# Optimization experiments

Measured on AMD Instinct MI355X. Metric: run time of the kernel, lower is better.

## Reference

```python
import jax, jax.numpy as jnp
import numpy as np

B, N, D = 4, 4096, 128
H = 128  # hidden_size == input_size (required by residual add)

def setup_inputs() -> dict:
    key = jax.random.key(0)
    kx, kw, kb = jax.random.split(key, 3)
    x = jax.random.normal(kx, (B, N, D), dtype=jnp.float32)
    # nn.Linear(input_size, hidden_size): weight [H, D], bias [H]
    lim = 1.0 / np.sqrt(D)
    W = jax.random.uniform(kw, (H, D), dtype=jnp.float32, minval=-lim, maxval=lim)
    b = jax.random.uniform(kb, (H,), dtype=jnp.float32, minval=-lim, maxval=lim)
    return {"x": x, "W": W, "b": b}

def reference(x, W, b):
    # adj[b,i,j] = <x[b,i], x[b,j]>, relu
    adj = jax.nn.relu(jnp.einsum('bid,bjd->bij', x, x))  # [B,N,N]
    # torch sums over dim=1 (rows) -> per-column sums, then divides columns
    col_sum = adj.sum(axis=1)                 # [B,N]
    adj = adj / col_sum[:, None, :]           # broadcast over dim 1
    out = jnp.einsum('bij,bjd->bid', adj, x)  # aggregate
    out = jnp.tanh(jnp.einsum('bnd,hd->bnh', out, W) + b)
    # Dropout(0.5) treated as eval-mode identity
    return out + x  # residual=True
```

## Files before the change

kernel.cpp:

```cpp
#include <hip/hip_runtime.h>
#include <hip/hip_bf16.h>

#define BN 4
#define NN 4096
#define DD 128

typedef __attribute__((ext_vector_type(8))) __bf16 bf16x8;
typedef __attribute__((ext_vector_type(4))) float f32x4;

typedef union {
  bf16x8 v;
  unsigned int u[4];
  uint2 u2[2];
} pk8;

typedef __attribute__((address_space(1))) const unsigned int* gas_p;
typedef __attribute__((address_space(3))) unsigned int* las_p;

__device__ __forceinline__ void gload16(const void* g, void* l) {
  __builtin_amdgcn_global_load_lds((gas_p)g, (las_p)l, 16, 0, 0);
}
__device__ __forceinline__ void wait_vm0() {
  asm volatile("s_waitcnt vmcnt(0)" ::: "memory");
}
__device__ __forceinline__ void wait_vm4() {
  asm volatile("s_waitcnt vmcnt(4)" ::: "memory");
}
__device__ __forceinline__ unsigned int cvtpk(float lo, float hi) {
  unsigned int r;
  asm("v_cvt_pk_bf16_f32 %0, %1, %2" : "=v"(r) : "v"(lo), "v"(hi));
  return r;
}
__device__ __forceinline__ unsigned int pkrelu(float lo, float hi) {
  return cvtpk(fmaxf(lo, 0.f), fmaxf(hi, 0.f));
}

__device__ inline unsigned short f2bf(float f) {
  unsigned int u = __float_as_uint(f);
  unsigned int r = (u + 0x7FFFu + ((u >> 16) & 1u)) >> 16;
  return (unsigned short)r;
}
__device__ inline float bf2f(unsigned short s) {
  return __uint_as_float(((unsigned int)s) << 16);
}

__global__ __launch_bounds__(256) void k_cvt(const float* __restrict__ x,
                                             unsigned short* __restrict__ xb) {
  int i = (blockIdx.x * 256 + threadIdx.x) * 8;
  float4 a = *(const float4*)(x + i);
  float4 c = *(const float4*)(x + i + 4);
  uint4 o;
  o.x = cvtpk(a.x, a.y);
  o.y = cvtpk(a.z, a.w);
  o.z = cvtpk(c.x, c.y);
  o.w = cvtpk(c.z, c.w);
  *(uint4*)(xb + i) = o;
}

__global__ __launch_bounds__(256, 4) void k_colsum(const unsigned short* __restrict__ xb,
                                                   float* __restrict__ colpart) {
  __shared__ unsigned short XiB[2][64 * 128];
  const int b = blockIdx.y, j0 = blockIdx.x * 128, ic = blockIdx.z;
  const int tid = threadIdx.x, lane = tid & 63, wv = tid >> 6;
  const unsigned short* xbb = xb + b * NN * DD;
  const int g = lane >> 4;
  const int ibeg = ic * (NN / 8);
  const int nt = (NN / 8) / 64;

#pragma unroll
  for (int hb = 0; hb < 2; ++hb)
#pragma unroll
    for (int q = 0; q < 4; ++q) {
      int c = wv * 4 + q;
      int lr = c * 4 + g;
      int gsrc = (lane & 15) ^ (lr & 7);
      gload16(&xbb[(j0 + hb * 64 + lr) * 128 + gsrc * 8], &XiB[hb][c * 512]);
    }
  wait_vm0();
  __syncthreads();

  bf16x8 bfr[2][4];
#pragma unroll
  for (int ni = 0; ni < 2; ++ni)
#pragma unroll
    for (int kk = 0; kk < 4; ++kk) {
      int lr = (wv & 1) * 32 + ni * 16 + (lane & 15);
      bfr[ni][kk] = *(const bf16x8*)&XiB[wv >> 1][lr * 128 + (((kk * 4 + g) ^ (lr & 7)) << 3)];
    }
  __syncthreads();

#pragma unroll
  for (int q = 0; q < 4; ++q) {
    int c = wv * 4 + q;
    int lr = c * 4 + g;
    int gsrc = (lane & 15) ^ (lr & 7);
    gload16(&xbb[(ibeg + lr) * 128 + gsrc * 8], &XiB[1][c * 512]);
  }

  int basek[4];
#pragma unroll
  for (int kk = 0; kk < 4; ++kk)
    basek[kk] = (lane & 15) * 128 + (((kk * 4 + g) ^ (lane & 7)) << 3);

  float colacc0 = 0.f, colacc1 = 0.f;
  for (int t = 0; t < nt; ++t) {
    wait_vm0();
    __syncthreads();
    const int cur = (t + 1) & 1, nxt = t & 1;
    if (t + 1 < nt) {
      const int i1 = ibeg + (t + 1) * 64;
#pragma unroll
      for (int q = 0; q < 4; ++q) {
        int c = wv * 4 + q;
        int lr = c * 4 + g;
        int gsrc = (lane & 15) ^ (lr & 7);
        gload16(&xbb[(i1 + lr) * 128 + gsrc * 8], &XiB[nxt][c * 512]);
      }
    }
    f32x4 a0[4], a1[4];
#pragma unroll
    for (int mj = 0; mj < 4; ++mj) { a0[mj] = (f32x4){}; a1[mj] = (f32x4){}; }
    __builtin_amdgcn_s_setprio(1);
#pragma unroll
    for (int kk = 0; kk < 4; ++kk) {
      bf16x8 ar0 = *(const bf16x8*)&XiB[cur][basek[kk]];
      bf16x8 ar1 = *(const bf16x8*)&XiB[cur][basek[kk] + 1 * 2048];
      bf16x8 ar2 = *(const bf16x8*)&XiB[cur][basek[kk] + 2 * 2048];
      bf16x8 ar3 = *(const bf16x8*)&XiB[cur][basek[kk] + 3 * 2048];
      a0[0] = __builtin_amdgcn_mfma_f32_16x16x32_bf16(ar0, bfr[0][kk], a0[0], 0, 0, 0);
      a1[0] = __builtin_amdgcn_mfma_f32_16x16x32_bf16(ar0, bfr[1][kk], a1[0], 0, 0, 0);
      a0[1] = __builtin_amdgcn_mfma_f32_16x16x32_bf16(ar1, bfr[0][kk], a0[1], 0, 0, 0);
      a1[1] = __builtin_amdgcn_mfma_f32_16x16x32_bf16(ar1, bfr[1][kk], a1[1], 0, 0, 0);
      a0[2] = __builtin_amdgcn_mfma_f32_16x16x32_bf16(ar2, bfr[0][kk], a0[2], 0, 0, 0);
      a1[2] = __builtin_amdgcn_mfma_f32_16x16x32_bf16(ar2, bfr[1][kk], a1[2], 0, 0, 0);
      a0[3] = __builtin_amdgcn_mfma_f32_16x16x32_bf16(ar3, bfr[0][kk], a0[3], 0, 0, 0);
      a1[3] = __builtin_amdgcn_mfma_f32_16x16x32_bf16(ar3, bfr[1][kk], a1[3], 0, 0, 0);
    }
    __builtin_amdgcn_s_setprio(0);
    {
      float s0 = 0.f, s1 = 0.f;
#pragma unroll
      for (int mj = 0; mj < 4; ++mj)
#pragma unroll
        for (int r = 0; r < 4; ++r) {
          s0 += fmaxf(a0[mj][r], 0.f);
          s1 += fmaxf(a1[mj][r], 0.f);
        }
      s0 += __shfl_xor(s0, 16); s0 += __shfl_xor(s0, 32);
      s1 += __shfl_xor(s1, 16); s1 += __shfl_xor(s1, 32);
      colacc0 += s0; colacc1 += s1;
    }
  }
  if (lane < 16) {
    colpart[(ic * BN + b) * NN + j0 + wv * 32 + lane] = colacc0;
    colpart[(ic * BN + b) * NN + j0 + wv * 32 + 16 + lane] = colacc1;
  }
}

__global__ __launch_bounds__(256) void k_ytrans(const float* __restrict__ x,
                                                const float* __restrict__ colpart,
                                                unsigned short* __restrict__ yt) {
  __shared__ unsigned short T[64 * 72];
  const int b = blockIdx.z, j0 = blockIdx.y * 64, d0 = blockIdx.x * 64;
  const int tid = threadIdx.x;
  int jr = tid >> 2, q0 = (tid & 3) * 16;
  float cs = 0.f;
#pragma unroll
  for (int ic = 0; ic < 8; ++ic) cs += colpart[(ic * BN + b) * NN + j0 + jr];
  float inv = 1.0f / cs;
  const float* xr = x + (size_t)(b * NN + j0 + jr) * DD + d0 + q0;
#pragma unroll
  for (int q = 0; q < 4; ++q) {
    float4 v = *(const float4*)(xr + q * 4);
    int dc = q0 + q * 4;
    T[jr * 72 + dc + 0] = f2bf(v.x * inv);
    T[jr * 72 + dc + 1] = f2bf(v.y * inv);
    T[jr * 72 + dc + 2] = f2bf(v.z * inv);
    T[jr * 72 + dc + 3] = f2bf(v.w * inv);
  }
  __syncthreads();
  for (int c = tid; c < 512; c += 256) {
    int dr = c >> 3, jg = c & 7;
    alignas(16) unsigned short tmp[8];
#pragma unroll
    for (int u = 0; u < 8; ++u) tmp[u] = T[(jg * 8 + u) * 72 + dr];
    *(uint4*)&yt[(size_t)(b * DD + d0 + dr) * NN + j0 + jg * 8] = *(const uint4*)tmp;
  }
}

__global__ __launch_bounds__(256, 2) void k_pass2(const unsigned short* __restrict__ xb,
                                                  const unsigned short* __restrict__ yt,
                                                  unsigned short* __restrict__ opart,
                                                  int jc) {
  __shared__ unsigned short XjB[2][64 * 128];
  __shared__ unsigned short YsB[3][128 * 64];
  const int b = blockIdx.y, i0 = blockIdx.x * 128, zc = blockIdx.z;
  const int tid = threadIdx.x, lane = tid & 63, wv = tid >> 6;
  const unsigned short* xbb = xb + b * NN * DD;
  const unsigned short* ytb = yt + (size_t)b * DD * NN;
  const int g = lane >> 4, l15 = lane & 15;

  const int jspan = NN / jc;
  const int jbeg = zc * jspan;
  const int nt = jspan / 64;

#pragma unroll
  for (int hb = 0; hb < 2; ++hb)
#pragma unroll
    for (int q = 0; q < 4; ++q) {
      int c = wv * 4 + q;
      int lr = c * 4 + g;
      int gsrc = l15 ^ (lr & 7);
      gload16(&xbb[(i0 + hb * 64 + lr) * 128 + gsrc * 8], &XjB[hb][c * 512]);
    }
  wait_vm0();
  __syncthreads();

  bf16x8 bfr[2][4];
#pragma unroll
  for (int ni = 0; ni < 2; ++ni)
#pragma unroll
    for (int kk = 0; kk < 4; ++kk) {
      int lr = (wv & 1) * 32 + ni * 16 + l15;
      bfr[ni][kk] = *(const bf16x8*)&XjB[wv >> 1][lr * 128 + (((kk * 4 + g) ^ (lr & 7)) << 3)];
    }
  __syncthreads();

#pragma unroll
  for (int q = 0; q < 4; ++q) {
    int c = wv * 4 + q;
    int lr = c * 4 + g;
    int gsrc = l15 ^ (lr & 7);
    gload16(&xbb[(jbeg + lr) * 128 + gsrc * 8], &XjB[0][c * 512]);
  }
#pragma unroll
  for (int q = 0; q < 4; ++q) {
    int c = wv * 4 + q;
    int dr = c * 8 + (lane >> 3);
    int gsrc = (lane & 7) ^ (dr & 7);
    gload16(&ytb[(size_t)dr * NN + jbeg + gsrc * 8], &YsB[0][c * 512]);
  }
  if (1 < nt) {
#pragma unroll
    for (int q = 0; q < 4; ++q) {
      int c = wv * 4 + q;
      int dr = c * 8 + (lane >> 3);
      int gsrc = (lane & 7) ^ (dr & 7);
      gload16(&ytb[(size_t)dr * NN + jbeg + 64 + gsrc * 8], &YsB[1][c * 512]);
    }
  }

  int xjb[4];
#pragma unroll
  for (int kk = 0; kk < 4; ++kk)
    xjb[kk] = l15 * 128 + (((kk * 4 + g) ^ (lane & 7)) << 3);
  int ysb[2][2];
#pragma unroll
  for (int c = 0; c < 2; ++c)
#pragma unroll
    for (int h = 0; h < 2; ++h) {
      int jq = c * 4 + 2 * h + (g >> 1);
      ysb[c][h] = l15 * 64 + ((jq ^ (l15 & 7)) << 3) + (g & 1) * 4;
    }

  f32x4 oacc0[8], oacc1[8];
#pragma unroll
  for (int n = 0; n < 8; ++n) { oacc0[n] = (f32x4){}; oacc1[n] = (f32x4){}; }

  int ybuf = 0;
  for (int t = 0; t < nt; ++t) {
    if (t + 1 < nt) wait_vm4(); else wait_vm0();
    __syncthreads();
    if (t + 1 < nt) {
      const int j1 = jbeg + (t + 1) * 64;
#pragma unroll
      for (int q = 0; q < 4; ++q) {
        int c = wv * 4 + q;
        int lr = c * 4 + g;
        int gsrc = l15 ^ (lr & 7);
        gload16(&xbb[(j1 + lr) * 128 + gsrc * 8], &XjB[(t + 1) & 1][c * 512]);
      }
      if (t + 2 < nt) {
        const int j2 = jbeg + (t + 2) * 64;
        int nb = ybuf + 2; if (nb >= 3) nb -= 3;
#pragma unroll
        for (int q = 0; q < 4; ++q) {
          int c = wv * 4 + q;
          int dr = c * 8 + (lane >> 3);
          int gsrc = (lane & 7) ^ (dr & 7);
          gload16(&ytb[(size_t)dr * NN + j2 + gsrc * 8], &YsB[nb][c * 512]);
        }
      }
    }
    const unsigned short* Xj = XjB[t & 1];
    const unsigned short* Ys = YsB[ybuf];

    f32x4 s0[4], s1[4];
#pragma unroll
    for (int mj = 0; mj < 4; ++mj) { s0[mj] = (f32x4){}; s1[mj] = (f32x4){}; }
    __builtin_amdgcn_s_setprio(1);
#pragma unroll
    for (int kk = 0; kk < 4; ++kk) {
      bf16x8 ar0 = *(const bf16x8*)&Xj[xjb[kk]];
      bf16x8 ar1 = *(const bf16x8*)&Xj[xjb[kk] + 1 * 2048];
      bf16x8 ar2 = *(const bf16x8*)&Xj[xjb[kk] + 2 * 2048];
      bf16x8 ar3 = *(const bf16x8*)&Xj[xjb[kk] + 3 * 2048];
      s0[0] = __builtin_amdgcn_mfma_f32_16x16x32_bf16(ar0, bfr[0][kk], s0[0], 0, 0, 0);
      s1[0] = __builtin_amdgcn_mfma_f32_16x16x32_bf16(ar0, bfr[1][kk], s1[0], 0, 0, 0);
      s0[1] = __builtin_amdgcn_mfma_f32_16x16x32_bf16(ar1, bfr[0][kk], s0[1], 0, 0, 0);
      s1[1] = __builtin_amdgcn_mfma_f32_16x16x32_bf16(ar1, bfr[1][kk], s1[1], 0, 0, 0);
      s0[2] = __builtin_amdgcn_mfma_f32_16x16x32_bf16(ar2, bfr[0][kk], s0[2], 0, 0, 0);
      s1[2] = __builtin_amdgcn_mfma_f32_16x16x32_bf16(ar2, bfr[1][kk], s1[2], 0, 0, 0);
      s0[3] = __builtin_amdgcn_mfma_f32_16x16x32_bf16(ar3, bfr[0][kk], s0[3], 0, 0, 0);
      s1[3] = __builtin_amdgcn_mfma_f32_16x16x32_bf16(ar3, bfr[1][kk], s1[3], 0, 0, 0);
    }
    __builtin_amdgcn_s_setprio(0);
    pk8 p00, p01, p10, p11;
    p00.u[0] = pkrelu(s0[0][0], s0[0][1]); p00.u[1] = pkrelu(s0[0][2], s0[0][3]);
    p00.u[2] = pkrelu(s0[1][0], s0[1][1]); p00.u[3] = pkrelu(s0[1][2], s0[1][3]);
    p01.u[0] = pkrelu(s1[0][0], s1[0][1]); p01.u[1] = pkrelu(s1[0][2], s1[0][3]);
    p01.u[2] = pkrelu(s1[1][0], s1[1][1]); p01.u[3] = pkrelu(s1[1][2], s1[1][3]);
    p10.u[0] = pkrelu(s0[2][0], s0[2][1]); p10.u[1] = pkrelu(s0[2][2], s0[2][3]);
    p10.u[2] = pkrelu(s0[3][0], s0[3][1]); p10.u[3] = pkrelu(s0[3][2], s0[3][3]);
    p11.u[0] = pkrelu(s1[2][0], s1[2][1]); p11.u[1] = pkrelu(s1[2][2], s1[2][3]);
    p11.u[2] = pkrelu(s1[3][0], s1[3][1]); p11.u[3] = pkrelu(s1[3][2], s1[3][3]);
    __builtin_amdgcn_s_setprio(1);
#pragma unroll
    for (int n = 0; n < 8; ++n) {
      pk8 bb0, bb1;
      bb0.u2[0] = *(const uint2*)&Ys[ysb[0][0] + n * 1024];
      bb0.u2[1] = *(const uint2*)&Ys[ysb[0][1] + n * 1024];
      bb1.u2[0] = *(const uint2*)&Ys[ysb[1][0] + n * 1024];
      bb1.u2[1] = *(const uint2*)&Ys[ysb[1][1] + n * 1024];
      oacc0[n] = __builtin_amdgcn_mfma_f32_16x16x32_bf16(p00.v, bb0.v, oacc0[n], 0, 0, 0);
      oacc1[n] = __builtin_amdgcn_mfma_f32_16x16x32_bf16(p01.v, bb0.v, oacc1[n], 0, 0, 0);
      oacc0[n] = __builtin_amdgcn_mfma_f32_16x16x32_bf16(p10.v, bb1.v, oacc0[n], 0, 0, 0);
      oacc1[n] = __builtin_amdgcn_mfma_f32_16x16x32_bf16(p11.v, bb1.v, oacc1[n], 0, 0, 0);
    }
    __builtin_amdgcn_s_setprio(0);
    ++ybuf; if (ybuf == 3) ybuf = 0;
  }

  __syncthreads();
  unsigned short* sb = &XjB[0][0];
#pragma unroll
  for (int m = 0; m < 2; ++m)
#pragma unroll
    for (int n = 0; n < 8; ++n)
#pragma unroll
      for (int r = 0; r < 4; ++r) {
        int row = wv * 32 + m * 16 + g * 4 + r;
        int col = n * 16 + l15;
        sb[row * 128 + col] = f2bf(m == 0 ? oacc0[n][r] : oacc1[n][r]);
      }
  __syncthreads();
  for (int c = tid; c < 2048; c += 256) {
    int row = c >> 4, gq = c & 15;
    *(uint4*)&opart[((size_t)zc * (BN * NN) + b * NN + i0 + row) * DD + gq * 8] =
        *(const uint4*)&sb[row * 128 + gq * 8];
  }
}

__global__ __launch_bounds__(256) void k_final(const unsigned short* __restrict__ opart,
                                               int jc,
                                               const float* __restrict__ W,
                                               const float* __restrict__ bias,
                                               const float* __restrict__ x,
                                               float* __restrict__ out) {
  __shared__ unsigned short Wb[128 * 128];
  __shared__ unsigned short PreS[32 * 128];
  const int tid = threadIdx.x, lane = tid & 63, wv = tid >> 6;
  const int g = lane >> 4;
  const int r0 = blockIdx.x * 32;

  {
    int h = tid >> 1, k0h = (tid & 1) * 8;
    const float* wr = W + h * 128 + k0h * 8;
#pragma unroll
    for (int q = 0; q < 8; ++q) {
      float4 v0 = *(const float4*)(wr + q * 8);
      float4 v1 = *(const float4*)(wr + q * 8 + 4);
      uint4 o;
      o.x = cvtpk(v0.x, v0.y); o.y = cvtpk(v0.z, v0.w);
      o.z = cvtpk(v1.x, v1.y); o.w = cvtpk(v1.z, v1.w);
      int gq = k0h + q;
      *(uint4*)&Wb[h * 128 + ((gq ^ (h & 7)) << 3)] = o;
    }
  }
  for (int c = tid; c < 512; c += 256) {
    int row = c >> 4, gq = c & 15;
    float s[8] = {0.f, 0.f, 0.f, 0.f, 0.f, 0.f, 0.f, 0.f};
    for (int ch = 0; ch < jc; ++ch) {
      uint4 pk = *(const uint4*)&opart[((size_t)ch * (BN * NN) + r0 + row) * DD + gq * 8];
      alignas(16) unsigned short us[8];
      *(uint4*)us = pk;
#pragma unroll
      for (int u = 0; u < 8; ++u) s[u] += bf2f(us[u]);
    }
    uint4 o;
    o.x = cvtpk(s[0], s[1]); o.y = cvtpk(s[2], s[3]);
    o.z = cvtpk(s[4], s[5]); o.w = cvtpk(s[6], s[7]);
    *(uint4*)&PreS[row * 128 + ((gq ^ (row & 7)) << 3)] = o;
  }
  __syncthreads();

  bf16x8 af[2][4], bf[2][4];
#pragma unroll
  for (int m = 0; m < 2; ++m)
#pragma unroll
    for (int kk = 0; kk < 4; ++kk) {
      int row = m * 16 + (lane & 15);
      af[m][kk] = *(const bf16x8*)&PreS[row * 128 + (((kk * 4 + g) ^ (row & 7)) << 3)];
    }
#pragma unroll
  for (int n = 0; n < 2; ++n)
#pragma unroll
    for (int kk = 0; kk < 4; ++kk) {
      int h = wv * 32 + n * 16 + (lane & 15);
      bf[n][kk] = *(const bf16x8*)&Wb[h * 128 + (((kk * 4 + g) ^ (h & 7)) << 3)];
    }

  f32x4 acc[2][2] = {};
#pragma unroll
  for (int kk = 0; kk < 4; ++kk) {
    acc[0][0] = __builtin_amdgcn_mfma_f32_16x16x32_bf16(af[0][kk], bf[0][kk], acc[0][0], 0, 0, 0);
    acc[0][1] = __builtin_amdgcn_mfma_f32_16x16x32_bf16(af[0][kk], bf[1][kk], acc[0][1], 0, 0, 0);
    acc[1][0] = __builtin_amdgcn_mfma_f32_16x16x32_bf16(af[1][kk], bf[0][kk], acc[1][0], 0, 0, 0);
    acc[1][1] = __builtin_amdgcn_mfma_f32_16x16x32_bf16(af[1][kk], bf[1][kk], acc[1][1], 0, 0, 0);
  }

  float bh0 = bias[wv * 32 + (lane & 15)];
  float bh1 = bias[wv * 32 + 16 + (lane & 15)];
#pragma unroll
  for (int m = 0; m < 2; ++m)
#pragma unroll
    for (int n = 0; n < 2; ++n)
#pragma unroll
      for (int r = 0; r < 4; ++r) {
        int row = r0 + m * 16 + g * 4 + r;
        int h = wv * 32 + n * 16 + (lane & 15);
        size_t idx = (size_t)row * 128 + h;
        out[idx] = tanhf(acc[m][n][r] + (n == 0 ? bh0 : bh1)) + x[idx];
      }
}

extern "C" void kernel_launch(void* const* d_in, const int* in_sizes, int n_in,
                              void* d_out, int out_size, void* d_ws, size_t ws_size,
                              hipStream_t stream) {
  (void)in_sizes; (void)n_in; (void)out_size;
  const float* x = (const float*)d_in[0];
  const float* W = (const float*)d_in[1];
  const float* bias = (const float*)d_in[2];
  float* out = (float*)d_out;
  char* ws = (char*)d_ws;
  unsigned short* xb = (unsigned short*)ws;
  unsigned short* yt = (unsigned short*)(ws + (4u << 20));
  float* colpart = (float*)(ws + (8u << 20));
  unsigned short* opart = (unsigned short*)(ws + (9u << 20));

  const size_t need4 = (9u << 20) + 4u * (4u << 20);
  const int jc = (ws_size >= need4) ? 4 : 1;

  k_cvt<<<1024, 256, 0, stream>>>(x, xb);
  k_colsum<<<dim3(32, 4, 8), 256, 0, stream>>>(xb, colpart);
  k_ytrans<<<dim3(2, 64, 4), 256, 0, stream>>>(x, colpart, yt);
  k_pass2<<<dim3(32, 4, jc), 256, 0, stream>>>(xb, yt, opart, jc);
  k_final<<<512, 256, 0, stream>>>(opart, jc, W, bias, x, out);
}
```

Baseline: 83.55 us.

## Single-buffer Y tile via register prefetch and split j-range six ways

Shrinks the Y shared-memory staging from three buffers to one by reading the Y fragments into registers before issuing the next tile's load, which lowers LDS use per block and may allow more blocks per CU. The j-range split grows from 4 to 6 chunks when the workspace allows it, with uneven tile counts distributed across chunks, giving more blocks in the grid. Y loads are no longer prefetched two tiles ahead, so load latency is less hidden, and a full vmcnt(0) wait plus an extra barrier now run every iteration. The final reduction kernel also has more partials to combine.

```diff
diff --git a/kernel.cpp b/kernel.cpp
--- a/kernel.cpp
+++ b/kernel.cpp
@@ -22,9 +22,6 @@
 }
 __device__ __forceinline__ void wait_vm0() {
   asm volatile("s_waitcnt vmcnt(0)" ::: "memory");
-}
-__device__ __forceinline__ void wait_vm4() {
-  asm volatile("s_waitcnt vmcnt(4)" ::: "memory");
 }
 __device__ __forceinline__ unsigned int cvtpk(float lo, float hi) {
   unsigned int r;
@@ -193,16 +190,17 @@
                                                   unsigned short* __restrict__ opart,
                                                   int jc) {
   __shared__ unsigned short XjB[2][64 * 128];
-  __shared__ unsigned short YsB[3][128 * 64];
+  __shared__ unsigned short YsB[128 * 64];
   const int b = blockIdx.y, i0 = blockIdx.x * 128, zc = blockIdx.z;
   const int tid = threadIdx.x, lane = tid & 63, wv = tid >> 6;
   const unsigned short* xbb = xb + b * NN * DD;
   const unsigned short* ytb = yt + (size_t)b * DD * NN;
   const int g = lane >> 4, l15 = lane & 15;
 
-  const int jspan = NN / jc;
-  const int jbeg = zc * jspan;
-  const int nt = jspan / 64;
+  const int base = 64 / jc, rem = 64 % jc;
+  const int st = zc * base + (zc < rem ? zc : rem);
+  const int nt = base + (zc < rem ? 1 : 0);
+  const int jbeg = st * 64;
 
 #pragma unroll
   for (int hb = 0; hb < 2; ++hb)
@@ -238,22 +236,13 @@
     int c = wv * 4 + q;
     int dr = c * 8 + (lane >> 3);
     int gsrc = (lane & 7) ^ (dr & 7);
-    gload16(&ytb[(size_t)dr * NN + jbeg + gsrc * 8], &YsB[0][c * 512]);
-  }
-  if (1 < nt) {
-#pragma unroll
-    for (int q = 0; q < 4; ++q) {
-      int c = wv * 4 + q;
-      int dr = c * 8 + (lane >> 3);
-      int gsrc = (lane & 7) ^ (dr & 7);
-      gload16(&ytb[(size_t)dr * NN + jbeg + 64 + gsrc * 8], &YsB[1][c * 512]);
-    }
+    gload16(&ytb[(size_t)dr * NN + jbeg + gsrc * 8], &YsB[c * 512]);
   }
 
   int xjb[4];
 #pragma unroll
   for (int kk = 0; kk < 4; ++kk)
-    xjb[kk] = l15 * 128 + (((kk * 4 + g) ^ (lane & 7)) << 3);
+    xjb[kk] = l15 * 128 + (((kk * 4 + g) ^ (l15 & 7)) << 3);
   int ysb[2][2];
 #pragma unroll
   for (int c = 0; c < 2; ++c)
@@ -267,9 +256,8 @@
 #pragma unroll
   for (int n = 0; n < 8; ++n) { oacc0[n] = (f32x4){}; oacc1[n] = (f32x4){}; }
 
-  int ybuf = 0;
   for (int t = 0; t < nt; ++t) {
-    if (t + 1 < nt) wait_vm4(); else wait_vm0();
+    wait_vm0();
     __syncthreads();
     if (t + 1 < nt) {
       const int j1 = jbeg + (t + 1) * 64;
@@ -280,20 +268,8 @@
         int gsrc = l15 ^ (lr & 7);
         gload16(&xbb[(j1 + lr) * 128 + gsrc * 8], &XjB[(t + 1) & 1][c * 512]);
       }
-      if (t + 2 < nt) {
-        const int j2 = jbeg + (t + 2) * 64;
-        int nb = ybuf + 2; if (nb >= 3) nb -= 3;
-#pragma unroll
-        for (int q = 0; q < 4; ++q) {
-          int c = wv * 4 + q;
-          int dr = c * 8 + (lane >> 3);
-          int gsrc = (lane & 7) ^ (dr & 7);
-          gload16(&ytb[(size_t)dr * NN + j2 + gsrc * 8], &YsB[nb][c * 512]);
-        }
-      }
     }
     const unsigned short* Xj = XjB[t & 1];
-    const unsigned short* Ys = YsB[ybuf];
 
     f32x4 s0[4], s1[4];
 #pragma unroll
@@ -315,6 +291,27 @@
       s1[3] = __builtin_amdgcn_mfma_f32_16x16x32_bf16(ar3, bfr[1][kk], s1[3], 0, 0, 0);
     }
     __builtin_amdgcn_s_setprio(0);
+
+    pk8 yf[8][2];
+#pragma unroll
+    for (int n = 0; n < 8; ++n)
+#pragma unroll
+      for (int c2 = 0; c2 < 2; ++c2) {
+        yf[n][c2].u2[0] = *(const uint2*)&YsB[ysb[c2][0] + n * 1024];
+        yf[n][c2].u2[1] = *(const uint2*)&YsB[ysb[c2][1] + n * 1024];
+      }
+    __syncthreads();
+    if (t + 1 < nt) {
+      const int j1 = jbeg + (t + 1) * 64;
+#pragma unroll
+      for (int q = 0; q < 4; ++q) {
+        int c = wv * 4 + q;
+        int dr = c * 8 + (lane >> 3);
+        int gsrc = (lane & 7) ^ (dr & 7);
+        gload16(&ytb[(size_t)dr * NN + j1 + gsrc * 8], &YsB[c * 512]);
+      }
+    }
+
     pk8 p00, p01, p10, p11;
     p00.u[0] = pkrelu(s0[0][0], s0[0][1]); p00.u[1] = pkrelu(s0[0][2], s0[0][3]);
     p00.u[2] = pkrelu(s0[1][0], s0[1][1]); p00.u[3] = pkrelu(s0[1][2], s0[1][3]);
@@ -327,18 +324,12 @@
     __builtin_amdgcn_s_setprio(1);
 #pragma unroll
     for (int n = 0; n < 8; ++n) {
-      pk8 bb0, bb1;
-      bb0.u2[0] = *(const uint2*)&Ys[ysb[0][0] + n * 1024];
-      bb0.u2[1] = *(const uint2*)&Ys[ysb[0][1] + n * 1024];
-      bb1.u2[0] = *(const uint2*)&Ys[ysb[1][0] + n * 1024];
-      bb1.u2[1] = *(const uint2*)&Ys[ysb[1][1] + n * 1024];
-      oacc0[n] = __builtin_amdgcn_mfma_f32_16x16x32_bf16(p00.v, bb0.v, oacc0[n], 0, 0, 0);
-      oacc1[n] = __builtin_amdgcn_mfma_f32_16x16x32_bf16(p01.v, bb0.v, oacc1[n], 0, 0, 0);
-      oacc0[n] = __builtin_amdgcn_mfma_f32_16x16x32_bf16(p10.v, bb1.v, oacc0[n], 0, 0, 0);
-      oacc1[n] = __builtin_amdgcn_mfma_f32_16x16x32_bf16(p11.v, bb1.v, oacc1[n], 0, 0, 0);
+      oacc0[n] = __builtin_amdgcn_mfma_f32_16x16x32_bf16(p00.v, yf[n][0].v, oacc0[n], 0, 0, 0);
+      oacc1[n] = __builtin_amdgcn_mfma_f32_16x16x32_bf16(p01.v, yf[n][0].v, oacc1[n], 0, 0, 0);
+      oacc0[n] = __builtin_amdgcn_mfma_f32_16x16x32_bf16(p10.v, yf[n][1].v, oacc0[n], 0, 0, 0);
+      oacc1[n] = __builtin_amdgcn_mfma_f32_16x16x32_bf16(p11.v, yf[n][1].v, oacc1[n], 0, 0, 0);
     }
     __builtin_amdgcn_s_setprio(0);
-    ++ybuf; if (ybuf == 3) ybuf = 0;
   }
 
   __syncthreads();
@@ -458,8 +449,9 @@
   float* colpart = (float*)(ws + (8u << 20));
   unsigned short* opart = (unsigned short*)(ws + (9u << 20));
 
+  const size_t need6 = (9u << 20) + 6u * (4u << 20);
   const size_t need4 = (9u << 20) + 4u * (4u << 20);
-  const int jc = (ws_size >= need4) ? 4 : 1;
+  const int jc = (ws_size >= need6) ? 6 : (ws_size >= need4) ? 4 : 1;
 
   k_cvt<<<1024, 256, 0, stream>>>(x, xb);
   k_colsum<<<dim3(32, 4, 8), 256, 0, stream>>>(xb, colpart);
```

Measured after the change: 95.31 us. +14.1%, slower.

## Double pass2 block to 512 threads over 256 rows and split j into 8 chunks

Applied to the files above, without the earlier changes.

k_pass2 now runs 8 waves per block, each owning 32 query rows, so one block covers 256 rows. The streamed Xj and Y tiles are shared across twice as many waves, and each thread issues half as many async loads. The per-wave query fragments are now loaded straight from global memory instead of staged through LDS. The j dimension is split into 8 chunks when the workspace is large enough, which keeps the grid size up. The costs are more partial outputs for k_final to reduce, a 4-blocks-per-CU launch bound that may limit registers per thread, and LDS occupancy that may not allow that many blocks.

```diff
diff --git a/kernel.cpp b/kernel.cpp
--- a/kernel.cpp
+++ b/kernel.cpp
@@ -23,8 +23,8 @@
 __device__ __forceinline__ void wait_vm0() {
   asm volatile("s_waitcnt vmcnt(0)" ::: "memory");
 }
-__device__ __forceinline__ void wait_vm4() {
-  asm volatile("s_waitcnt vmcnt(4)" ::: "memory");
+__device__ __forceinline__ void wait_vm2() {
+  asm volatile("s_waitcnt vmcnt(2)" ::: "memory");
 }
 __device__ __forceinline__ unsigned int cvtpk(float lo, float hi) {
   unsigned int r;
@@ -188,13 +188,13 @@
   }
 }
 
-__global__ __launch_bounds__(256, 2) void k_pass2(const unsigned short* __restrict__ xb,
+__global__ __launch_bounds__(512, 4) void k_pass2(const unsigned short* __restrict__ xb,
                                                   const unsigned short* __restrict__ yt,
                                                   unsigned short* __restrict__ opart,
                                                   int jc) {
   __shared__ unsigned short XjB[2][64 * 128];
   __shared__ unsigned short YsB[3][128 * 64];
-  const int b = blockIdx.y, i0 = blockIdx.x * 128, zc = blockIdx.z;
+  const int b = blockIdx.y, i0 = blockIdx.x * 256, zc = blockIdx.z;
   const int tid = threadIdx.x, lane = tid & 63, wv = tid >> 6;
   const unsigned short* xbb = xb + b * NN * DD;
   const unsigned short* ytb = yt + (size_t)b * DD * NN;
@@ -204,46 +204,32 @@
   const int jbeg = zc * jspan;
   const int nt = jspan / 64;
 
-#pragma unroll
-  for (int hb = 0; hb < 2; ++hb)
-#pragma unroll
-    for (int q = 0; q < 4; ++q) {
-      int c = wv * 4 + q;
-      int lr = c * 4 + g;
-      int gsrc = l15 ^ (lr & 7);
-      gload16(&xbb[(i0 + hb * 64 + lr) * 128 + gsrc * 8], &XjB[hb][c * 512]);
-    }
-  wait_vm0();
-  __syncthreads();
-
   bf16x8 bfr[2][4];
 #pragma unroll
   for (int ni = 0; ni < 2; ++ni)
 #pragma unroll
-    for (int kk = 0; kk < 4; ++kk) {
-      int lr = (wv & 1) * 32 + ni * 16 + l15;
-      bfr[ni][kk] = *(const bf16x8*)&XjB[wv >> 1][lr * 128 + (((kk * 4 + g) ^ (lr & 7)) << 3)];
-    }
-  __syncthreads();
-
-#pragma unroll
-  for (int q = 0; q < 4; ++q) {
-    int c = wv * 4 + q;
+    for (int kk = 0; kk < 4; ++kk)
+      bfr[ni][kk] = *(const bf16x8*)&xbb[(size_t)(i0 + wv * 32 + ni * 16 + l15) * 128 +
+                                         (kk * 4 + g) * 8];
+
+#pragma unroll
+  for (int q = 0; q < 2; ++q) {
+    int c = wv * 2 + q;
     int lr = c * 4 + g;
     int gsrc = l15 ^ (lr & 7);
     gload16(&xbb[(jbeg + lr) * 128 + gsrc * 8], &XjB[0][c * 512]);
   }
 #pragma unroll
-  for (int q = 0; q < 4; ++q) {
-    int c = wv * 4 + q;
+  for (int q = 0; q < 2; ++q) {
+    int c = wv * 2 + q;
     int dr = c * 8 + (lane >> 3);
     int gsrc = (lane & 7) ^ (dr & 7);
     gload16(&ytb[(size_t)dr * NN + jbeg + gsrc * 8], &YsB[0][c * 512]);
   }
   if (1 < nt) {
 #pragma unroll
-    for (int q = 0; q < 4; ++q) {
-      int c = wv * 4 + q;
+    for (int q = 0; q < 2; ++q) {
+      int c = wv * 2 + q;
       int dr = c * 8 + (lane >> 3);
       int gsrc = (lane & 7) ^ (dr & 7);
       gload16(&ytb[(size_t)dr * NN + jbeg + 64 + gsrc * 8], &YsB[1][c * 512]);
@@ -253,7 +239,7 @@
   int xjb[4];
 #pragma unroll
   for (int kk = 0; kk < 4; ++kk)
-    xjb[kk] = l15 * 128 + (((kk * 4 + g) ^ (lane & 7)) << 3);
+    xjb[kk] = l15 * 128 + (((kk * 4 + g) ^ (l15 & 7)) << 3);
   int ysb[2][2];
 #pragma unroll
   for (int c = 0; c < 2; ++c)
@@ -269,13 +255,13 @@
 
   int ybuf = 0;
   for (int t = 0; t < nt; ++t) {
-    if (t + 1 < nt) wait_vm4(); else wait_vm0();
+    if (t + 1 < nt) wait_vm2(); else wait_vm0();
     __syncthreads();
     if (t + 1 < nt) {
       const int j1 = jbeg + (t + 1) * 64;
 #pragma unroll
-      for (int q = 0; q < 4; ++q) {
-        int c = wv * 4 + q;
+      for (int q = 0; q < 2; ++q) {
+        int c = wv * 2 + q;
         int lr = c * 4 + g;
         int gsrc = l15 ^ (lr & 7);
         gload16(&xbb[(j1 + lr) * 128 + gsrc * 8], &XjB[(t + 1) & 1][c * 512]);
@@ -284,8 +270,8 @@
         const int j2 = jbeg + (t + 2) * 64;
         int nb = ybuf + 2; if (nb >= 3) nb -= 3;
 #pragma unroll
-        for (int q = 0; q < 4; ++q) {
-          int c = wv * 4 + q;
+        for (int q = 0; q < 2; ++q) {
+          int c = wv * 2 + q;
           int dr = c * 8 + (lane >> 3);
           int gsrc = (lane & 7) ^ (dr & 7);
           gload16(&ytb[(size_t)dr * NN + j2 + gsrc * 8], &YsB[nb][c * 512]);
@@ -342,22 +328,25 @@
   }
 
   __syncthreads();
-  unsigned short* sb = &XjB[0][0];
+  unsigned short* sb = (wv < 4) ? &XjB[0][0] : &YsB[0][0];
+  const int rb = (wv & 3) * 32;
 #pragma unroll
   for (int m = 0; m < 2; ++m)
 #pragma unroll
     for (int n = 0; n < 8; ++n)
 #pragma unroll
       for (int r = 0; r < 4; ++r) {
-        int row = wv * 32 + m * 16 + g * 4 + r;
+        int row = rb + m * 16 + g * 4 + r;
         int col = n * 16 + l15;
         sb[row * 128 + col] = f2bf(m == 0 ? oacc0[n][r] : oacc1[n][r]);
       }
   __syncthreads();
-  for (int c = tid; c < 2048; c += 256) {
+  for (int c = tid; c < 4096; c += 512) {
     int row = c >> 4, gq = c & 15;
+    const unsigned short* src = (row < 128) ? &XjB[0][row * 128 + gq * 8]
+                                            : &YsB[0][(row - 128) * 128 + gq * 8];
     *(uint4*)&opart[((size_t)zc * (BN * NN) + b * NN + i0 + row) * DD + gq * 8] =
-        *(const uint4*)&sb[row * 128 + gq * 8];
+        *(const uint4*)src;
   }
 }
 
@@ -458,12 +447,13 @@
   float* colpart = (float*)(ws + (8u << 20));
   unsigned short* opart = (unsigned short*)(ws + (9u << 20));
 
+  const size_t need8 = (9u << 20) + 8u * (4u << 20);
   const size_t need4 = (9u << 20) + 4u * (4u << 20);
-  const int jc = (ws_size >= need4) ? 4 : 1;
+  const int jc = (ws_size >= need8) ? 8 : (ws_size >= need4) ? 4 : 1;
 
   k_cvt<<<1024, 256, 0, stream>>>(x, xb);
   k_colsum<<<dim3(32, 4, 8), 256, 0, stream>>>(xb, colpart);
   k_ytrans<<<dim3(2, 64, 4), 256, 0, stream>>>(x, colpart, yt);
-  k_pass2<<<dim3(32, 4, jc), 256, 0, stream>>>(xb, yt, opart, jc);
+  k_pass2<<<dim3(16, 4, jc), 512, 0, stream>>>(xb, yt, opart, jc);
   k_final<<<512, 256, 0, stream>>>(opart, jc, W, bias, x, out);
 }
```

New measurement: 119.0 us. +42.5%, slower.
